# Kernel optimization log

Measured on AMD Instinct MI355X. Metric: run time of the kernel, lower is better.

Reference implementation:

```python
import jax, jax.numpy as jnp
import numpy as np

V = 196608   # HEALPix nside=128 -> 12*128^2 pixels
NNZ = 1769472  # ~9 entries per row (8 neighbors + diagonal)
B = 4
P = 64
Q = 64
K = 3  # KERNEL_SIZE


def setup_inputs() -> dict:
    key = jax.random.key(0)
    ks = jax.random.split(key, 5)
    return {
        "lap_vals": jax.random.normal(ks[0], (NNZ,), jnp.float32) * 0.1,
        "x": jax.random.normal(ks[1], (B, V, P), jnp.float32),
        "weight": jax.random.normal(ks[2], (K, P, Q), jnp.float32) * 0.1,
        "bias": jnp.full((Q,), 0.01, jnp.float32),
        "lap_rows": jax.random.randint(ks[3], (NNZ,), 0, V, jnp.int32),
        "lap_cols": jax.random.randint(ks[4], (NNZ,), 0, V, jnp.int32),
    }


def _spmm(vals, rows, cols, x):
    # sparse [V,V] @ dense [V,M] via gather + segment_sum
    return jax.ops.segment_sum(vals[:, None] * x[cols], rows, num_segments=V)


def reference(lap_vals, x, weight, bias, lap_rows, lap_cols):
    Bb, Vv, Pp = x.shape
    Kk, _, Qq = weight.shape
    # x0: [V, P*B] as in torch permute(1,2,0).view
    x0 = x.transpose(1, 2, 0).reshape(Vv, Pp * Bb)
    x1 = _spmm(lap_vals, lap_rows, lap_cols, x0)
    x2 = 2.0 * _spmm(lap_vals, lap_rows, lap_cols, x1) - x0
    cheb = jnp.stack([x0, x1, x2], 0).reshape(Kk, Vv, Pp, Bb)  # [K,V,P,B]
    inp = cheb.transpose(3, 1, 2, 0).reshape(Bb * Vv, Pp * Kk)  # [B*V, P*K]
    # NOTE: weight [K,P,Q] flattened C-order to [K*P, Q], matching torch .view
    out = inp @ weight.reshape(Kk * Pp, Qq)
    return out.reshape(Bb, Vv, Qq) + bias
```

## Files before the change

### kernel.cpp

```cpp
#include <hip/hip_runtime.h>
#include <hip/hip_bf16.h>

#define Vn   196608
#define NNZn 1769472
#define Bn   4
#define Pn   64
#define Qn   64
#define VPn  (Vn*Pn)
#define NB   256
#define RPB  768
#define EPT  4096
#define NTIL 432

typedef __hip_bfloat16 bf16;
typedef __attribute__((ext_vector_type(8))) short bf16x8;
typedef __attribute__((ext_vector_type(4))) float f32x4;
typedef __attribute__((ext_vector_type(4))) unsigned int u32x4;

__device__ inline short f2bs(float f){
  __hip_bfloat16 h = __float2bfloat16(f);
  return *(short*)&h;
}
__device__ inline float lo16(unsigned u){ return __uint_as_float(u<<16); }
__device__ inline float hi16(unsigned u){ return __uint_as_float(u & 0xffff0000u); }

__global__ void k_zero256(unsigned* __restrict__ g){ g[threadIdx.x] = 0u; }


__global__ __launch_bounds__(256) void k_pre(const int* __restrict__ rows, unsigned* __restrict__ gcount,
                      const float* __restrict__ x, short* __restrict__ x0c,
                      const float* __restrict__ wf, short* __restrict__ wcb){
  __shared__ unsigned hcnt[NB];
  const int bid = blockIdx.x, t = threadIdx.x;
  if(bid % 58 == 0){
    const int cb = bid/58;
    hcnt[t] = 0u;
    __syncthreads();
    const int base = cb*EPT;
#pragma unroll
    for(int k=0;k<4;++k){
      const int4 r = *(const int4*)(rows + base + k*1024 + t*4);
      atomicAdd(&hcnt[(unsigned)r.x/RPB], 1u);
      atomicAdd(&hcnt[(unsigned)r.y/RPB], 1u);
      atomicAdd(&hcnt[(unsigned)r.z/RPB], 1u);
      atomicAdd(&hcnt[(unsigned)r.w/RPB], 1u);
    }
    __syncthreads();
    atomicAdd(&gcount[t], hcnt[t]);
    return;
  }
  const int f = bid - bid/58 - 1;
  if(f < 24576){
    const int i = f*256 + t;
    const int o = i*8;
    const int v = o>>8, bp = o&255;
    const int hh = bp>>7, w7 = bp&127;
    const int b = (hh<<1) + (w7>>6), p = w7&63;
    const float* xp = x + (size_t)b*VPn + (size_t)v*64 + p;
    const float4 f0 = *(const float4*)xp;
    const float4 f1 = *(const float4*)(xp+4);
    unsigned r0 = ((unsigned)(unsigned short)f2bs(f0.y)<<16) | (unsigned)(unsigned short)f2bs(f0.x);
    unsigned r1 = ((unsigned)(unsigned short)f2bs(f0.w)<<16) | (unsigned)(unsigned short)f2bs(f0.z);
    unsigned r2 = ((unsigned)(unsigned short)f2bs(f1.y)<<16) | (unsigned)(unsigned short)f2bs(f1.x);
    unsigned r3 = ((unsigned)(unsigned short)f2bs(f1.w)<<16) | (unsigned)(unsigned short)f2bs(f1.z);
    u32x4 u; u[0]=r0; u[1]=r1; u[2]=r2; u[3]=r3;
    *(u32x4*)(x0c + ((size_t)hh*Vn + v)*128 + w7) = u;
  } else {
    const int idx = (f - 24576)*256 + t;
    const int q = idx/192, rem = idx%192, part = rem>>6, p = rem&63;
    float w;
    if(part==0)      w = wf[(3*p+0)*64+q] - wf[(3*p+2)*64+q];
    else if(part==1) w = wf[(3*p+1)*64+q];
    else             w = 2.0f*wf[(3*p+2)*64+q];
    wcb[idx] = f2bs(w);
  }
}

__global__ void k_scan256(const unsigned* __restrict__ gcount, unsigned* __restrict__ gbase,
                          unsigned* __restrict__ gcursor){
  __shared__ unsigned t[NB];
  const int i = threadIdx.x;
  const unsigned c = gcount[i];
  t[i] = c;
  __syncthreads();
  for(int off=1; off<NB; off<<=1){
    unsigned v = (i>=off) ? t[i-off] : 0u;
    __syncthreads();
    t[i] += v;
    __syncthreads();
  }
  const unsigned excl = t[i] - c;
  gbase[i] = excl;
  gcursor[i] = excl;
  if(i == NB-1) gbase[NB] = t[NB-1];
}

__global__ __launch_bounds__(256) void k_bucket(const int* __restrict__ rows, const int* __restrict__ cols,
                         const float* __restrict__ vals, unsigned* __restrict__ gcursor,
                         int* __restrict__ brow, int2* __restrict__ bmeta){
  __shared__ unsigned hcnt[NB];
  __shared__ unsigned lcur[NB];
  const int t = threadIdx.x;
  const int base = blockIdx.x*EPT;
  hcnt[t] = 0u;
  __syncthreads();
  int4 r4[4];
#pragma unroll
  for(int k=0;k<4;++k){
    r4[k] = *(const int4*)(rows + base + k*1024 + t*4);
    atomicAdd(&hcnt[(unsigned)r4[k].x/RPB], 1u);
    atomicAdd(&hcnt[(unsigned)r4[k].y/RPB], 1u);
    atomicAdd(&hcnt[(unsigned)r4[k].z/RPB], 1u);
    atomicAdd(&hcnt[(unsigned)r4[k].w/RPB], 1u);
  }
  __syncthreads();
  lcur[t] = atomicAdd(&gcursor[t], hcnt[t]);
  __syncthreads();
#pragma unroll
  for(int k=0;k<4;++k){
    const int4   c4 = *(const int4*)(cols + base + k*1024 + t*4);
    const float4 v4 = *(const float4*)(vals + base + k*1024 + t*4);
    unsigned p;
    p = atomicAdd(&lcur[(unsigned)r4[k].x/RPB],1u); brow[p]=r4[k].x; { int2 m; m.x=c4.x; m.y=__float_as_int(v4.x); bmeta[p]=m; }
    p = atomicAdd(&lcur[(unsigned)r4[k].y/RPB],1u); brow[p]=r4[k].y; { int2 m; m.x=c4.y; m.y=__float_as_int(v4.y); bmeta[p]=m; }
    p = atomicAdd(&lcur[(unsigned)r4[k].z/RPB],1u); brow[p]=r4[k].z; { int2 m; m.x=c4.z; m.y=__float_as_int(v4.z); bmeta[p]=m; }
    p = atomicAdd(&lcur[(unsigned)r4[k].w/RPB],1u); brow[p]=r4[k].w; { int2 m; m.x=c4.w; m.y=__float_as_int(v4.w); bmeta[p]=m; }
  }
}

__global__ __launch_bounds__(256) void k_csr(const int* __restrict__ brow, const int2* __restrict__ bmeta,
                      const unsigned* __restrict__ gbase,
                      unsigned* __restrict__ rstart, unsigned* __restrict__ rend,
                      int2* __restrict__ meta){
  __shared__ unsigned rcnt[RPB];
  __shared__ unsigned rcur[RPB];
  __shared__ unsigned ssum[256];
  const int t = threadIdx.x, b = blockIdx.x;
  const unsigned base = gbase[b];
  const int nb = (int)(gbase[b+1] - base);
  const int rv0 = b*RPB;
#pragma unroll
  for(int k=0;k<3;++k) rcnt[t*3+k] = 0u;
  __syncthreads();
  for(int e=t; e<nb; e+=256){
    const int r = brow[base+e] - rv0;
    atomicAdd(&rcnt[r], 1u);
  }
  __syncthreads();
  const unsigned c0 = rcnt[t*3], c1 = rcnt[t*3+1], c2 = rcnt[t*3+2];
  const unsigned mysum = c0+c1+c2;
  ssum[t] = mysum;
  __syncthreads();
  for(int off=1; off<256; off<<=1){
    unsigned v = (t>=off) ? ssum[t-off] : 0u;
    __syncthreads();
    ssum[t] += v;
    __syncthreads();
  }
  const unsigned excl = ssum[t] - mysum;
  const unsigned s0 = base + excl, s1 = s0 + c0, s2 = s1 + c1;
  rstart[rv0+t*3+0] = s0;  rend[rv0+t*3+0] = s0 + c0;  rcur[t*3+0] = s0;
  rstart[rv0+t*3+1] = s1;  rend[rv0+t*3+1] = s1 + c1;  rcur[t*3+1] = s1;
  rstart[rv0+t*3+2] = s2;  rend[rv0+t*3+2] = s2 + c2;  rcur[t*3+2] = s2;
  __syncthreads();
  for(int e=t; e<nb; e+=256){
    const int r = brow[base+e] - rv0;
    const unsigned pos = atomicAdd(&rcur[r], 1u);
    meta[pos] = bmeta[base+e];
  }
}


#define SP_STAGE(U,W,I) { int c_=0; float wv_=0.f; \
    if((I) < n){ const int2 m_ = meta[s+(unsigned)(I)]; c_=m_.x; wv_=__int_as_float(m_.y);} \
    W = wv_; U = *(const u32x4*)(src + (size_t)c_*SROW + off); }
#define SP_CONSUME(U,W) { \
    a0=fmaf(W,lo16(U[0]),a0); a1=fmaf(W,hi16(U[0]),a1); \
    a2=fmaf(W,lo16(U[1]),a2); a3=fmaf(W,hi16(U[1]),a3); \
    a4=fmaf(W,lo16(U[2]),a4); a5=fmaf(W,hi16(U[2]),a5); \
    a6=fmaf(W,lo16(U[3]),a6); a7=fmaf(W,hi16(U[3]),a7); }
#define SP_BODY \
  float a0=0,a1=0,a2=0,a3=0,a4=0,a5=0,a6=0,a7=0; \
  if(nmax > 0){ \
    u32x4 u0,u1,u2,u3; float w0,w1,w2,w3; \
    SP_STAGE(u0,w0,0) SP_STAGE(u1,w1,1) SP_STAGE(u2,w2,2) SP_STAGE(u3,w3,3) \
    int rem = nmax - 4; \
    int j = 4; \
    while(rem > 0){ \
      const u32x4 p0=u0, p1=u1, p2=u2, p3=u3; \
      const float q0=w0, q1=w1, q2=w2, q3=w3; \
      SP_STAGE(u0,w0,j) SP_STAGE(u1,w1,j+1) SP_STAGE(u2,w2,j+2) SP_STAGE(u3,w3,j+3) \
      SP_CONSUME(p0,q0) SP_CONSUME(p1,q1) SP_CONSUME(p2,q2) SP_CONSUME(p3,q3) \
      rem -= 4; j += 4; \
    } \
    SP_CONSUME(u0,w0) SP_CONSUME(u1,w1) SP_CONSUME(u2,w2) SP_CONSUME(u3,w3) \
  } \
  unsigned r0 = ((unsigned)(unsigned short)f2bs(a1)<<16) | (unsigned)(unsigned short)f2bs(a0); \
  unsigned r1 = ((unsigned)(unsigned short)f2bs(a3)<<16) | (unsigned)(unsigned short)f2bs(a2); \
  unsigned r2 = ((unsigned)(unsigned short)f2bs(a5)<<16) | (unsigned)(unsigned short)f2bs(a4); \
  unsigned r3 = ((unsigned)(unsigned short)f2bs(a7)<<16) | (unsigned)(unsigned short)f2bs(a6); \
  u32x4 ov; ov[0]=r0; ov[1]=r1; ov[2]=r2; ov[3]=r3;


template<int SROW, size_t PSTR>
__global__ __launch_bounds__(256) void k_spmm(const short* __restrict__ src,
                          const int2* __restrict__ meta,
                          const unsigned* __restrict__ rstart, const unsigned* __restrict__ rend,
                          short* __restrict__ dst){
  const int tid = threadIdx.x;
  const int lane = tid & 63;
  const int half = lane >> 5, sub = lane & 31;
  const int vbase = blockIdx.x*8 + (tid>>6)*2;
  const unsigned sA = rstart[vbase],   sB = rstart[vbase+1];
  const int nA = (int)(rend[vbase]-sA), nB = (int)(rend[vbase+1]-sB);
  const int nmax = (nA > nB) ? nA : nB;
  const unsigned s = half ? sB : sA;
  const int n = half ? nB : nA;
  const size_t off = (size_t)(sub>>4)*PSTR + (size_t)((sub&15)*8);
  SP_BODY
  *(u32x4*)(dst + (size_t)(vbase+half)*256 + sub*8) = ov;
}


__global__ __launch_bounds__(256) void k_gemm_fused(
    const short* __restrict__ x0, const short* __restrict__ x1,
    const short* __restrict__ wcb, const float* __restrict__ bias,
    const int2* __restrict__ meta, const unsigned* __restrict__ rstart,
    const unsigned* __restrict__ rend, float* __restrict__ out){
  __shared__ short ylds[4][16*264];
  const int t = threadIdx.x, w = t>>6, l = t&63;
  const int half = l>>5, sub = l&31;
  const int vw = blockIdx.x*64 + w*16;
  short* const my = &ylds[w][0];
  const short* const src = x1;
  const int SROW = 256;
  const size_t off = (size_t)(sub>>4)*128 + (size_t)((sub&15)*8);

  for(int pr=0; pr<8; ++pr){
    const int vb = vw + pr*2;
    const unsigned sA = rstart[vb], sB = rstart[vb+1];
    const int nA = (int)(rend[vb]-sA), nB = (int)(rend[vb+1]-sB);
    const int nmax = (nA > nB) ? nA : nB;
    const unsigned s = half ? sB : sA;
    const int n = half ? nB : nA;
    SP_BODY
    *(u32x4*)(my + (pr*2+half)*264 + off) = ov;
  }

  const int r = l&15, g = l>>4;
  f32x4 acc[4][4] = {};
#pragma unroll
  for(int c=0; c<6; ++c){
    const int part = c>>1, ko = (c&1)*32;
    const int kw = part*64 + ko + 8*g;
    const bf16x8 bfr0 = *(const bf16x8*)&wcb[( 0+r)*192 + kw];
    const bf16x8 bfr1 = *(const bf16x8*)&wcb[(16+r)*192 + kw];
    const bf16x8 bfr2 = *(const bf16x8*)&wcb[(32+r)*192 + kw];
    const bf16x8 bfr3 = *(const bf16x8*)&wcb[(48+r)*192 + kw];
#pragma unroll
    for(int bb=0; bb<4; ++bb){
      bf16x8 a;
      if(part==0)      a = *(const bf16x8*)(x0 + ((size_t)(bb>>1)*Vn + vw + r)*128 + (bb&1)*64 + ko + 8*g);
      else if(part==1) a = *(const bf16x8*)(x1 + ((size_t)(vw + r))*256 + bb*64 + ko + 8*g);
      else             a = *(const bf16x8*)(my + r*264 + bb*64 + ko + 8*g);
      acc[bb][0] = __builtin_amdgcn_mfma_f32_16x16x32_bf16(a, bfr0, acc[bb][0], 0, 0, 0);
      acc[bb][1] = __builtin_amdgcn_mfma_f32_16x16x32_bf16(a, bfr1, acc[bb][1], 0, 0, 0);
      acc[bb][2] = __builtin_amdgcn_mfma_f32_16x16x32_bf16(a, bfr2, acc[bb][2], 0, 0, 0);
      acc[bb][3] = __builtin_amdgcn_mfma_f32_16x16x32_bf16(a, bfr3, acc[bb][3], 0, 0, 0);
    }
  }

#pragma unroll
  for(int bb=0; bb<4; ++bb){
    float* ob = out + (size_t)bb*Vn*64;
#pragma unroll
    for(int n=0; n<4; ++n){
      const float bq = bias[n*16+r];
#pragma unroll
      for(int reg=0; reg<4; ++reg)
        ob[(size_t)(vw + g*4 + reg)*64 + n*16 + r] = acc[bb][n][reg] + bq;
    }
  }
}


extern "C" void kernel_launch(void* const* d_in, const int* in_sizes, int n_in,
                              void* d_out, int out_size, void* d_ws, size_t ws_size,
                              hipStream_t stream){
  const float* lap_vals = (const float*)d_in[0];
  const float* x        = (const float*)d_in[1];
  const float* weight   = (const float*)d_in[2];
  const float* bias     = (const float*)d_in[3];
  const int*   lap_rows = (const int*)d_in[4];
  const int*   lap_cols = (const int*)d_in[5];
  float* out = (float*)d_out;
  short* x0c = (short*)d_out;

  char* w = (char*)d_ws;
  short* x1b = (short*)w;          w += (size_t)Vn*256*sizeof(short);
  int2* meta = (int2*)w;           w += (size_t)NNZn*8;
  int2* bmeta = (int2*)w;          w += (size_t)NNZn*8;
  int*  brow = (int*)w;            w += (size_t)NNZn*4;
  unsigned* rstart = (unsigned*)w; w += (size_t)Vn*4;
  unsigned* rend   = (unsigned*)w; w += (size_t)Vn*4;
  unsigned* gcount = (unsigned*)w; w += NB*4;
  unsigned* gbase  = (unsigned*)w; w += (NB+1)*4;
  unsigned* gcursor= (unsigned*)w; w += NB*4;
  short* wcb = (short*)w;          w += 12288*sizeof(short);

  k_zero256<<<1, 256, 0, stream>>>(gcount);
  k_pre<<<25056, 256, 0, stream>>>(lap_rows, gcount, x, x0c, weight, wcb);
  k_scan256<<<1, 256, 0, stream>>>(gcount, gbase, gcursor);
  k_bucket<<<NTIL, 256, 0, stream>>>(lap_rows, lap_cols, lap_vals, gcursor, brow, bmeta);
  k_csr<<<NB, 256, 0, stream>>>(brow, bmeta, gbase, rstart, rend, meta);

  k_spmm<128, (size_t)Vn*128><<<Vn/8, 256, 0, stream>>>(x0c, meta, rstart, rend, x1b);

  k_gemm_fused<<<Vn/64, 256, 0, stream>>>(x0c, x1b, wcb, bias,
                                          meta, rstart, rend, out);
}
```

Baseline: 526.0 us.

## Split second SpMM into its own kernel and restructure the MFMA GEMM

The second Laplacian SpMM moves out of the fused GEMM kernel into a second launch of the standalone SpMM kernel, which writes y to a workspace buffer aliased over the now-dead bucket scratch. The SpMM kernel now has each wave process four rows, two independent accumulator sets, so more gathers are in flight per wave. The GEMM kernel stages the weights once in padded LDS, assigns one batch per wave with a 64-row M tile, and prefetches the next K-chunk of A while issuing MFMAs. In exchange, y makes an extra round trip through global memory and each SpMM thread holds more registers.

```diff
diff --git a/kernel.cpp b/kernel.cpp
--- a/kernel.cpp
+++ b/kernel.cpp
@@ -171,36 +171,25 @@
 }
 
 
-#define SP_STAGE(U,W,I) { int c_=0; float wv_=0.f; \
-    if((I) < n){ const int2 m_ = meta[s+(unsigned)(I)]; c_=m_.x; wv_=__int_as_float(m_.y);} \
+#define SP_STAGE2(U,W,I,S,N) { int c_=0; float wv_=0.f; \
+    if((I) < (N)){ const int2 m_ = meta[(S)+(unsigned)(I)]; c_=m_.x; wv_=__int_as_float(m_.y);} \
     W = wv_; U = *(const u32x4*)(src + (size_t)c_*SROW + off); }
-#define SP_CONSUME(U,W) { \
-    a0=fmaf(W,lo16(U[0]),a0); a1=fmaf(W,hi16(U[0]),a1); \
-    a2=fmaf(W,lo16(U[1]),a2); a3=fmaf(W,hi16(U[1]),a3); \
-    a4=fmaf(W,lo16(U[2]),a4); a5=fmaf(W,hi16(U[2]),a5); \
-    a6=fmaf(W,lo16(U[3]),a6); a7=fmaf(W,hi16(U[3]),a7); }
-#define SP_BODY \
-  float a0=0,a1=0,a2=0,a3=0,a4=0,a5=0,a6=0,a7=0; \
-  if(nmax > 0){ \
-    u32x4 u0,u1,u2,u3; float w0,w1,w2,w3; \
-    SP_STAGE(u0,w0,0) SP_STAGE(u1,w1,1) SP_STAGE(u2,w2,2) SP_STAGE(u3,w3,3) \
-    int rem = nmax - 4; \
-    int j = 4; \
-    while(rem > 0){ \
-      const u32x4 p0=u0, p1=u1, p2=u2, p3=u3; \
-      const float q0=w0, q1=w1, q2=w2, q3=w3; \
-      SP_STAGE(u0,w0,j) SP_STAGE(u1,w1,j+1) SP_STAGE(u2,w2,j+2) SP_STAGE(u3,w3,j+3) \
-      SP_CONSUME(p0,q0) SP_CONSUME(p1,q1) SP_CONSUME(p2,q2) SP_CONSUME(p3,q3) \
-      rem -= 4; j += 4; \
-    } \
-    SP_CONSUME(u0,w0) SP_CONSUME(u1,w1) SP_CONSUME(u2,w2) SP_CONSUME(u3,w3) \
-  } \
-  unsigned r0 = ((unsigned)(unsigned short)f2bs(a1)<<16) | (unsigned)(unsigned short)f2bs(a0); \
-  unsigned r1 = ((unsigned)(unsigned short)f2bs(a3)<<16) | (unsigned)(unsigned short)f2bs(a2); \
-  unsigned r2 = ((unsigned)(unsigned short)f2bs(a5)<<16) | (unsigned)(unsigned short)f2bs(a4); \
-  unsigned r3 = ((unsigned)(unsigned short)f2bs(a7)<<16) | (unsigned)(unsigned short)f2bs(a6); \
-  u32x4 ov; ov[0]=r0; ov[1]=r1; ov[2]=r2; ov[3]=r3;
-
+#define CONS_A(U,W) { \
+    aA0=fmaf(W,lo16(U[0]),aA0); aA1=fmaf(W,hi16(U[0]),aA1); \
+    aA2=fmaf(W,lo16(U[1]),aA2); aA3=fmaf(W,hi16(U[1]),aA3); \
+    aA4=fmaf(W,lo16(U[2]),aA4); aA5=fmaf(W,hi16(U[2]),aA5); \
+    aA6=fmaf(W,lo16(U[3]),aA6); aA7=fmaf(W,hi16(U[3]),aA7); }
+#define CONS_B(U,W) { \
+    aB0=fmaf(W,lo16(U[0]),aB0); aB1=fmaf(W,hi16(U[0]),aB1); \
+    aB2=fmaf(W,lo16(U[1]),aB2); aB3=fmaf(W,hi16(U[1]),aB3); \
+    aB4=fmaf(W,lo16(U[2]),aB4); aB5=fmaf(W,hi16(U[2]),aB5); \
+    aB6=fmaf(W,lo16(U[3]),aB6); aB7=fmaf(W,hi16(U[3]),aB7); }
+#define SP_PACK(OV,A0,A1,A2,A3,A4,A5,A6,A7) \
+  { unsigned t0 = ((unsigned)(unsigned short)f2bs(A1)<<16) | (unsigned)(unsigned short)f2bs(A0); \
+    unsigned t1 = ((unsigned)(unsigned short)f2bs(A3)<<16) | (unsigned)(unsigned short)f2bs(A2); \
+    unsigned t2 = ((unsigned)(unsigned short)f2bs(A5)<<16) | (unsigned)(unsigned short)f2bs(A4); \
+    unsigned t3 = ((unsigned)(unsigned short)f2bs(A7)<<16) | (unsigned)(unsigned short)f2bs(A6); \
+    OV[0]=t0; OV[1]=t1; OV[2]=t2; OV[3]=t3; }
 
 template<int SROW, size_t PSTR>
 __global__ __launch_bounds__(256) void k_spmm(const short* __restrict__ src,
@@ -210,75 +199,111 @@
   const int tid = threadIdx.x;
   const int lane = tid & 63;
   const int half = lane >> 5, sub = lane & 31;
-  const int vbase = blockIdx.x*8 + (tid>>6)*2;
-  const unsigned sA = rstart[vbase],   sB = rstart[vbase+1];
-  const int nA = (int)(rend[vbase]-sA), nB = (int)(rend[vbase+1]-sB);
-  const int nmax = (nA > nB) ? nA : nB;
-  const unsigned s = half ? sB : sA;
-  const int n = half ? nB : nA;
+  const int vbase = blockIdx.x*16 + (tid>>6)*4;
+  const unsigned sA0 = rstart[vbase],   sA1 = rstart[vbase+1];
+  const unsigned sB0 = rstart[vbase+2], sB1 = rstart[vbase+3];
+  const int nA0 = (int)(rend[vbase]-sA0),   nA1 = (int)(rend[vbase+1]-sA1);
+  const int nB0 = (int)(rend[vbase+2]-sB0), nB1 = (int)(rend[vbase+3]-sB1);
+  const int nmaxA = (nA0>nA1)?nA0:nA1, nmaxB = (nB0>nB1)?nB0:nB1;
+  const int T = (nmaxA>nmaxB)?nmaxA:nmaxB;
+  const unsigned sA = half ? sA1 : sA0;  const int nA = half ? nA1 : nA0;
+  const unsigned sB = half ? sB1 : sB0;  const int nB = half ? nB1 : nB0;
   const size_t off = (size_t)(sub>>4)*PSTR + (size_t)((sub&15)*8);
-  SP_BODY
-  *(u32x4*)(dst + (size_t)(vbase+half)*256 + sub*8) = ov;
-}
-
-
-__global__ __launch_bounds__(256) void k_gemm_fused(
-    const short* __restrict__ x0, const short* __restrict__ x1,
-    const short* __restrict__ wcb, const float* __restrict__ bias,
-    const int2* __restrict__ meta, const unsigned* __restrict__ rstart,
-    const unsigned* __restrict__ rend, float* __restrict__ out){
-  __shared__ short ylds[4][16*264];
-  const int t = threadIdx.x, w = t>>6, l = t&63;
-  const int half = l>>5, sub = l&31;
-  const int vw = blockIdx.x*64 + w*16;
-  short* const my = &ylds[w][0];
-  const short* const src = x1;
-  const int SROW = 256;
-  const size_t off = (size_t)(sub>>4)*128 + (size_t)((sub&15)*8);
-
-  for(int pr=0; pr<8; ++pr){
-    const int vb = vw + pr*2;
-    const unsigned sA = rstart[vb], sB = rstart[vb+1];
-    const int nA = (int)(rend[vb]-sA), nB = (int)(rend[vb+1]-sB);
-    const int nmax = (nA > nB) ? nA : nB;
-    const unsigned s = half ? sB : sA;
-    const int n = half ? nB : nA;
-    SP_BODY
-    *(u32x4*)(my + (pr*2+half)*264 + off) = ov;
-  }
-
-  const int r = l&15, g = l>>4;
+  float aA0=0,aA1=0,aA2=0,aA3=0,aA4=0,aA5=0,aA6=0,aA7=0;
+  float aB0=0,aB1=0,aB2=0,aB3=0,aB4=0,aB5=0,aB6=0,aB7=0;
+  if(T > 0){
+    u32x4 uA0,uA1,uA2,uA3, uB0,uB1,uB2,uB3;
+    float wA0,wA1,wA2,wA3, wB0,wB1,wB2,wB3;
+    SP_STAGE2(uA0,wA0,0,sA,nA) SP_STAGE2(uB0,wB0,0,sB,nB)
+    SP_STAGE2(uA1,wA1,1,sA,nA) SP_STAGE2(uB1,wB1,1,sB,nB)
+    SP_STAGE2(uA2,wA2,2,sA,nA) SP_STAGE2(uB2,wB2,2,sB,nB)
+    SP_STAGE2(uA3,wA3,3,sA,nA) SP_STAGE2(uB3,wB3,3,sB,nB)
+    int rem = T - 4, j = 4;
+    while(rem > 0){
+      const u32x4 pA0=uA0,pA1=uA1,pA2=uA2,pA3=uA3;
+      const float qA0=wA0,qA1=wA1,qA2=wA2,qA3=wA3;
+      const u32x4 pB0=uB0,pB1=uB1,pB2=uB2,pB3=uB3;
+      const float qB0=wB0,qB1=wB1,qB2=wB2,qB3=wB3;
+      SP_STAGE2(uA0,wA0,j,sA,nA)   SP_STAGE2(uB0,wB0,j,sB,nB)
+      SP_STAGE2(uA1,wA1,j+1,sA,nA) SP_STAGE2(uB1,wB1,j+1,sB,nB)
+      SP_STAGE2(uA2,wA2,j+2,sA,nA) SP_STAGE2(uB2,wB2,j+2,sB,nB)
+      SP_STAGE2(uA3,wA3,j+3,sA,nA) SP_STAGE2(uB3,wB3,j+3,sB,nB)
+      CONS_A(pA0,qA0) CONS_A(pA1,qA1) CONS_A(pA2,qA2) CONS_A(pA3,qA3)
+      CONS_B(pB0,qB0) CONS_B(pB1,qB1) CONS_B(pB2,qB2) CONS_B(pB3,qB3)
+      rem -= 4; j += 4;
+    }
+    CONS_A(uA0,wA0) CONS_A(uA1,wA1) CONS_A(uA2,wA2) CONS_A(uA3,wA3)
+    CONS_B(uB0,wB0) CONS_B(uB1,wB1) CONS_B(uB2,wB2) CONS_B(uB3,wB3)
+  }
+  u32x4 ovA, ovB;
+  SP_PACK(ovA,aA0,aA1,aA2,aA3,aA4,aA5,aA6,aA7)
+  SP_PACK(ovB,aB0,aB1,aB2,aB3,aB4,aB5,aB6,aB7)
+  *(u32x4*)(dst + (size_t)(vbase+half)*256 + sub*8) = ovA;
+  *(u32x4*)(dst + (size_t)(vbase+2+half)*256 + sub*8) = ovB;
+}
+
+
+#define WTP 200
+
+#define LOADA(dst, cc) { \
+  const int part_ = (cc)>>1, ko_ = ((cc)&1)*32; \
+  if(part_==0){ \
+    const short* sp = x0 + ((size_t)(w>>1)*Vn + v0 + r)*128 + (w&1)*64 + ko_ + 8*g; \
+    _Pragma("unroll") for(int m_=0;m_<4;++m_) dst[m_] = *(const bf16x8*)(sp + (size_t)m_*16*128); \
+  } else { \
+    const short* sp = (part_==1 ? x1 : y) + ((v0 + r)*256 + w*64 + ko_ + 8*g); \
+    _Pragma("unroll") for(int m_=0;m_<4;++m_) dst[m_] = *(const bf16x8*)(sp + (size_t)m_*16*256); \
+  } }
+
+__global__ __launch_bounds__(256) void k_gemm_mfma(const short* __restrict__ x0,
+                      const short* __restrict__ x1, const short* __restrict__ y,
+                      const short* __restrict__ wcb, const float* __restrict__ bias,
+                      float* __restrict__ out){
+  __shared__ short WT[64*WTP];
+  const int t = threadIdx.x;
+  for(int idx=t; idx<1536; idx+=256){
+    const int row = idx/24, ch = idx%24;
+    *(uint4*)&WT[row*WTP + ch*8] = ((const uint4*)wcb)[row*24 + ch];
+  }
+  const int w = t>>6;
+  const int l = t&63, r = l&15, g = l>>4;
+  const size_t v0 = (size_t)blockIdx.x*64;
   f32x4 acc[4][4] = {};
+  bf16x8 aC[4], aN[4];
+  LOADA(aC, 0);
+  __syncthreads();
+
 #pragma unroll
   for(int c=0; c<6; ++c){
+    if(c < 5) LOADA(aN, c+1);
     const int part = c>>1, ko = (c&1)*32;
     const int kw = part*64 + ko + 8*g;
-    const bf16x8 bfr0 = *(const bf16x8*)&wcb[( 0+r)*192 + kw];
-    const bf16x8 bfr1 = *(const bf16x8*)&wcb[(16+r)*192 + kw];
-    const bf16x8 bfr2 = *(const bf16x8*)&wcb[(32+r)*192 + kw];
-    const bf16x8 bfr3 = *(const bf16x8*)&wcb[(48+r)*192 + kw];
-#pragma unroll
-    for(int bb=0; bb<4; ++bb){
-      bf16x8 a;
-      if(part==0)      a = *(const bf16x8*)(x0 + ((size_t)(bb>>1)*Vn + vw + r)*128 + (bb&1)*64 + ko + 8*g);
-      else if(part==1) a = *(const bf16x8*)(x1 + ((size_t)(vw + r))*256 + bb*64 + ko + 8*g);
-      else             a = *(const bf16x8*)(my + r*264 + bb*64 + ko + 8*g);
-      acc[bb][0] = __builtin_amdgcn_mfma_f32_16x16x32_bf16(a, bfr0, acc[bb][0], 0, 0, 0);
-      acc[bb][1] = __builtin_amdgcn_mfma_f32_16x16x32_bf16(a, bfr1, acc[bb][1], 0, 0, 0);
-      acc[bb][2] = __builtin_amdgcn_mfma_f32_16x16x32_bf16(a, bfr2, acc[bb][2], 0, 0, 0);
-      acc[bb][3] = __builtin_amdgcn_mfma_f32_16x16x32_bf16(a, bfr3, acc[bb][3], 0, 0, 0);
-    }
-  }
-
-#pragma unroll
-  for(int bb=0; bb<4; ++bb){
-    float* ob = out + (size_t)bb*Vn*64;
-#pragma unroll
-    for(int n=0; n<4; ++n){
-      const float bq = bias[n*16+r];
-#pragma unroll
-      for(int reg=0; reg<4; ++reg)
-        ob[(size_t)(vw + g*4 + reg)*64 + n*16 + r] = acc[bb][n][reg] + bq;
+#pragma unroll
+    for(int n=0;n<4;++n){
+      const bf16x8 bfr = *(const bf16x8*)&WT[(n*16+r)*WTP + kw];
+#pragma unroll
+      for(int m=0;m<4;++m)
+        acc[m][n] = __builtin_amdgcn_mfma_f32_16x16x32_bf16(aC[m], bfr, acc[m][n], 0, 0, 0);
+    }
+    if(c < 5){
+#pragma unroll
+      for(int m=0;m<4;++m) aC[m] = aN[m];
+    }
+  }
+
+  __syncthreads();
+
+  float* ob = out + (size_t)w*Vn*64 + v0*64;
+#pragma unroll
+  for(int n=0;n<4;++n){
+    const float bq = bias[n*16+r];
+#pragma unroll
+    for(int m=0;m<4;++m){
+#pragma unroll
+      for(int reg=0;reg<4;++reg){
+        const int row = m*16 + g*4 + reg;
+        ob[(size_t)row*64 + n*16 + r] = acc[m][n][reg] + bq;
+      }
     }
   }
 }
@@ -299,8 +324,10 @@
   char* w = (char*)d_ws;
   short* x1b = (short*)w;          w += (size_t)Vn*256*sizeof(short);
   int2* meta = (int2*)w;           w += (size_t)NNZn*8;
-  int2* bmeta = (int2*)w;          w += (size_t)NNZn*8;
-  int*  brow = (int*)w;            w += (size_t)NNZn*4;
+  char* uni = w;                   w += (size_t)Vn*256*sizeof(short);
+  int2* bmeta = (int2*)uni;
+  int*  brow  = (int*)(uni + (size_t)NNZn*8);
+  short* yb   = (short*)uni;
   unsigned* rstart = (unsigned*)w; w += (size_t)Vn*4;
   unsigned* rend   = (unsigned*)w; w += (size_t)Vn*4;
   unsigned* gcount = (unsigned*)w; w += NB*4;
@@ -314,8 +341,8 @@
   k_bucket<<<NTIL, 256, 0, stream>>>(lap_rows, lap_cols, lap_vals, gcursor, brow, bmeta);
   k_csr<<<NB, 256, 0, stream>>>(brow, bmeta, gbase, rstart, rend, meta);
 
-  k_spmm<128, (size_t)Vn*128><<<Vn/8, 256, 0, stream>>>(x0c, meta, rstart, rend, x1b);
-
-  k_gemm_fused<<<Vn/64, 256, 0, stream>>>(x0c, x1b, wcb, bias,
-                                          meta, rstart, rend, out);
-}
+  k_spmm<128, (size_t)Vn*128><<<Vn/16, 256, 0, stream>>>(x0c, meta, rstart, rend, x1b);
+  k_spmm<256, 128><<<Vn/16, 256, 0, stream>>>(x1b, meta, rstart, rend, yb);
+
+  k_gemm_mfma<<<Vn/64, 256, 0, stream>>>(x0c, x1b, yb, wcb, bias, out);
+}
```

After: 569.4 us. +8.3%, slower.

## Unfuse second SpMM from GEMM and stage weights in LDS with prefetch

Applied to the files above, without the earlier changes.

Moves the second sparse product out of the GEMM kernel into its own k_spmm launch that writes to a workspace buffer aliased over the bucket scratch. The GEMM kernel then only does dense MFMA work: it stages the combined weights in padded shared memory, maps each wave to one batch, and double-buffers the A-fragment loads across K chunks. This trades an extra full write and read of the intermediate for better occupancy and simpler, latency-hidden GEMM loads.

```diff
diff --git a/kernel.cpp b/kernel.cpp
--- a/kernel.cpp
+++ b/kernel.cpp
@@ -201,7 +201,6 @@
   unsigned r3 = ((unsigned)(unsigned short)f2bs(a7)<<16) | (unsigned)(unsigned short)f2bs(a6); \
   u32x4 ov; ov[0]=r0; ov[1]=r1; ov[2]=r2; ov[3]=r3;
 
-
 template<int SROW, size_t PSTR>
 __global__ __launch_bounds__(256) void k_spmm(const short* __restrict__ src,
                           const int2* __restrict__ meta,
@@ -222,63 +221,67 @@
 }
 
 
-__global__ __launch_bounds__(256) void k_gemm_fused(
-    const short* __restrict__ x0, const short* __restrict__ x1,
-    const short* __restrict__ wcb, const float* __restrict__ bias,
-    const int2* __restrict__ meta, const unsigned* __restrict__ rstart,
-    const unsigned* __restrict__ rend, float* __restrict__ out){
-  __shared__ short ylds[4][16*264];
-  const int t = threadIdx.x, w = t>>6, l = t&63;
-  const int half = l>>5, sub = l&31;
-  const int vw = blockIdx.x*64 + w*16;
-  short* const my = &ylds[w][0];
-  const short* const src = x1;
-  const int SROW = 256;
-  const size_t off = (size_t)(sub>>4)*128 + (size_t)((sub&15)*8);
-
-  for(int pr=0; pr<8; ++pr){
-    const int vb = vw + pr*2;
-    const unsigned sA = rstart[vb], sB = rstart[vb+1];
-    const int nA = (int)(rend[vb]-sA), nB = (int)(rend[vb+1]-sB);
-    const int nmax = (nA > nB) ? nA : nB;
-    const unsigned s = half ? sB : sA;
-    const int n = half ? nB : nA;
-    SP_BODY
-    *(u32x4*)(my + (pr*2+half)*264 + off) = ov;
-  }
-
-  const int r = l&15, g = l>>4;
+#define WTP 200
+
+#define LOADA(dst, cc) { \
+  const int part_ = (cc)>>1, ko_ = ((cc)&1)*32; \
+  if(part_==0){ \
+    const short* sp = x0 + ((size_t)(w>>1)*Vn + v0 + r)*128 + (w&1)*64 + ko_ + 8*g; \
+    _Pragma("unroll") for(int m_=0;m_<4;++m_) dst[m_] = *(const bf16x8*)(sp + (size_t)m_*16*128); \
+  } else { \
+    const short* sp = (part_==1 ? x1 : y) + ((v0 + r)*256 + w*64 + ko_ + 8*g); \
+    _Pragma("unroll") for(int m_=0;m_<4;++m_) dst[m_] = *(const bf16x8*)(sp + (size_t)m_*16*256); \
+  } }
+
+__global__ __launch_bounds__(256) void k_gemm_mfma(const short* __restrict__ x0,
+                      const short* __restrict__ x1, const short* __restrict__ y,
+                      const short* __restrict__ wcb, const float* __restrict__ bias,
+                      float* __restrict__ out){
+  __shared__ short WT[64*WTP];
+  const int t = threadIdx.x;
+  for(int idx=t; idx<1536; idx+=256){
+    const int row = idx/24, ch = idx%24;
+    *(uint4*)&WT[row*WTP + ch*8] = ((const uint4*)wcb)[row*24 + ch];
+  }
+  const int w = t>>6;
+  const int l = t&63, r = l&15, g = l>>4;
+  const size_t v0 = (size_t)blockIdx.x*64;
   f32x4 acc[4][4] = {};
+  bf16x8 aC[4], aN[4];
+  LOADA(aC, 0);
+  __syncthreads();
+
 #pragma unroll
   for(int c=0; c<6; ++c){
+    if(c < 5) LOADA(aN, c+1);
     const int part = c>>1, ko = (c&1)*32;
     const int kw = part*64 + ko + 8*g;
-    const bf16x8 bfr0 = *(const bf16x8*)&wcb[( 0+r)*192 + kw];
-    const bf16x8 bfr1 = *(const bf16x8*)&wcb[(16+r)*192 + kw];
-    const bf16x8 bfr2 = *(const bf16x8*)&wcb[(32+r)*192 + kw];
-    const bf16x8 bfr3 = *(const bf16x8*)&wcb[(48+r)*192 + kw];
-#pragma unroll
-    for(int bb=0; bb<4; ++bb){
-      bf16x8 a;
-      if(part==0)      a = *(const bf16x8*)(x0 + ((size_t)(bb>>1)*Vn + vw + r)*128 + (bb&1)*64 + ko + 8*g);
-      else if(part==1) a = *(const bf16x8*)(x1 + ((size_t)(vw + r))*256 + bb*64 + ko + 8*g);
-      else             a = *(const bf16x8*)(my + r*264 + bb*64 + ko + 8*g);
-      acc[bb][0] = __builtin_amdgcn_mfma_f32_16x16x32_bf16(a, bfr0, acc[bb][0], 0, 0, 0);
-      acc[bb][1] = __builtin_amdgcn_mfma_f32_16x16x32_bf16(a, bfr1, acc[bb][1], 0, 0, 0);
-      acc[bb][2] = __builtin_amdgcn_mfma_f32_16x16x32_bf16(a, bfr2, acc[bb][2], 0, 0, 0);
-      acc[bb][3] = __builtin_amdgcn_mfma_f32_16x16x32_bf16(a, bfr3, acc[bb][3], 0, 0, 0);
+#pragma unroll
+    for(int n=0;n<4;++n){
+      const bf16x8 bfr = *(const bf16x8*)&WT[(n*16+r)*WTP + kw];
+#pragma unroll
+      for(int m=0;m<4;++m)
+        acc[m][n] = __builtin_amdgcn_mfma_f32_16x16x32_bf16(aC[m], bfr, acc[m][n], 0, 0, 0);
     }
-  }
-
-#pragma unroll
-  for(int bb=0; bb<4; ++bb){
-    float* ob = out + (size_t)bb*Vn*64;
-#pragma unroll
-    for(int n=0; n<4; ++n){
-      const float bq = bias[n*16+r];
-#pragma unroll
-      for(int reg=0; reg<4; ++reg)
-        ob[(size_t)(vw + g*4 + reg)*64 + n*16 + r] = acc[bb][n][reg] + bq;
+    if(c < 5){
+#pragma unroll
+      for(int m=0;m<4;++m) aC[m] = aN[m];
+    }
+  }
+
+  __syncthreads();
+
+  float* ob = out + (size_t)w*Vn*64 + v0*64;
+#pragma unroll
+  for(int n=0;n<4;++n){
+    const float bq = bias[n*16+r];
+#pragma unroll
+    for(int m=0;m<4;++m){
+#pragma unroll
+      for(int reg=0;reg<4;++reg){
+        const int row = m*16 + g*4 + reg;
+        ob[(size_t)row*64 + n*16 + r] = acc[m][n][reg] + bq;
+      }
     }
   }
 }
@@ -299,8 +302,10 @@
   char* w = (char*)d_ws;
   short* x1b = (short*)w;          w += (size_t)Vn*256*sizeof(short);
   int2* meta = (int2*)w;           w += (size_t)NNZn*8;
-  int2* bmeta = (int2*)w;          w += (size_t)NNZn*8;
-  int*  brow = (int*)w;            w += (size_t)NNZn*4;
+  char* uni = w;                   w += (size_t)Vn*256*sizeof(short);
+  int2* bmeta = (int2*)uni;
+  int*  brow  = (int*)(uni + (size_t)NNZn*8);
+  short* yb   = (short*)uni;
   unsigned* rstart = (unsigned*)w; w += (size_t)Vn*4;
   unsigned* rend   = (unsigned*)w; w += (size_t)Vn*4;
   unsigned* gcount = (unsigned*)w; w += NB*4;
@@ -315,7 +320,7 @@
   k_csr<<<NB, 256, 0, stream>>>(brow, bmeta, gbase, rstart, rend, meta);
 
   k_spmm<128, (size_t)Vn*128><<<Vn/8, 256, 0, stream>>>(x0c, meta, rstart, rend, x1b);
-
-  k_gemm_fused<<<Vn/64, 256, 0, stream>>>(x0c, x1b, wcb, bias,
-                                          meta, rstart, rend, out);
-}
+  k_spmm<256, 128><<<Vn/8, 256, 0, stream>>>(x1b, meta, rstart, rend, yb);
+
+  k_gemm_mfma<<<Vn/64, 256, 0, stream>>>(x0c, x1b, yb, wcb, bias, out);
+}
```

Result: faster. 511.8 us (-2.7%).
